# Performance work log

Measured on AMD Instinct MI355X. Metric: run time of the kernel, lower is better.

The kernel has to match this reference:

```python
import jax, jax.numpy as jnp
import numpy as np

B, N = 4, 1024
DIM, DEPTH, HEADS, DHEAD, MLP = 512, 6, 8, 64, 2048
INNER = HEADS * DHEAD
SCALE = DHEAD ** -0.5
EPS = 1e-5


def setup_inputs() -> dict:
    key = jax.random.key(0)
    ks = jax.random.split(key, 16)
    w = lambda k, shape: (jax.random.normal(k, shape, jnp.float32) * 0.02)
    D = DEPTH
    return {
        "g": jax.random.normal(ks[0], (B, N, DIM), jnp.float32),
        "x": jax.random.normal(ks[1], (B, N, DIM), jnp.float32),
        # PreNorm + SelfAttention
        "ln1_s": jnp.ones((D, DIM)), "ln1_b": jnp.zeros((D, DIM)),
        "Wqkv": w(ks[2], (D, DIM, 3 * INNER)),
        "Wo_sa": w(ks[3], (D, INNER, DIM)), "bo_sa": jnp.zeros((D, DIM)),
        # RelationalCrossAttention
        "lng_s": jnp.ones((D, DIM)), "lng_b": jnp.zeros((D, DIM)),
        "lnx_s": jnp.ones((D, DIM)), "lnx_b": jnp.zeros((D, DIM)),
        "Wq": w(ks[4], (D, DIM, INNER)),
        "Wk": w(ks[5], (D, DIM, INNER)),
        "Wv": w(ks[6], (D, DIM, INNER)), "bv": jnp.zeros((D, INNER)),
        "Wo_ca": w(ks[7], (D, INNER, DIM)), "bo_ca": jnp.zeros((D, DIM)),
        # PreNorm + FeedForward (same module applied twice per layer)
        "lnf_s": jnp.ones((D, DIM)), "lnf_b": jnp.zeros((D, DIM)),
        "W1": w(ks[8], (D, DIM, MLP)), "b1": jnp.zeros((D, MLP)),
        "W2": w(ks[9], (D, MLP, DIM)), "b2": jnp.zeros((D, DIM)),
    }


def _ln(t, s, b):
    m = t.mean(-1, keepdims=True)
    v = ((t - m) ** 2).mean(-1, keepdims=True)
    return (t - m) / jnp.sqrt(v + EPS) * s + b


def _split_heads(t):  # [b, n, h*d] -> [b, h, n, d]
    b, n, _ = t.shape
    return t.reshape(b, n, HEADS, DHEAD).transpose(0, 2, 1, 3)


def _merge_heads(t):  # [b, h, n, d] -> [b, n, h*d]
    b, h, n, d = t.shape
    return t.transpose(0, 2, 1, 3).reshape(b, n, h * d)


def _attend(q, k, v):
    dots = jnp.einsum('bhnd,bhmd->bhnm', q, k) * SCALE
    attn = jax.nn.softmax(jnp.nan_to_num(dots, nan=-jnp.inf), axis=-1)
    attn = jnp.nan_to_num(attn)  # nan_to_num(0.0) post-softmax as in source
    return jnp.einsum('bhnm,bhmd->bhnd', attn, jnp.nan_to_num(v))


def reference(g, x, ln1_s, ln1_b, Wqkv, Wo_sa, bo_sa, lng_s, lng_b, lnx_s, lnx_b,
              Wq, Wk, Wv, bv, Wo_ca, bo_ca, lnf_s, lnf_b, W1, b1, W2, b2):
    for i in range(DEPTH):
        def ff(t):
            h = jax.nn.gelu(_ln(t, lnf_s[i], lnf_b[i]) @ W1[i] + b1[i], approximate=False)
            return h @ W2[i] + b2[i]
        # relational cross attention: q,k from g, v from x
        gn = _ln(g, lng_s[i], lng_b[i])
        xn = _ln(x, lnx_s[i], lnx_b[i])
        q = _split_heads(gn @ Wq[i])
        k = _split_heads(gn @ Wk[i])
        v = _split_heads(xn @ Wv[i] + bv[i])
        x = _merge_heads(_attend(q, k, v)) @ Wo_ca[i] + bo_ca[i] + x
        x = ff(x) + x
        # pre-norm self attention (skip connection enabled)
        sn = _ln(x, ln1_s[i], ln1_b[i])
        qkv = sn @ Wqkv[i]
        qs, ks_, vs = jnp.split(qkv, 3, axis=-1)
        sa = _merge_heads(_attend(_split_heads(qs), _split_heads(ks_), _split_heads(vs)))
        x = sa @ Wo_sa[i] + bo_sa[i] + x
        x = ff(x) + x
    return x
```

## Files before the change

### kernel.cpp

```cpp
#include <hip/hip_runtime.h>
#include <hip/hip_bf16.h>
#include <cstdint>
#include <cstddef>

#define DEV __device__ __forceinline__

using f32x4 = __attribute__((ext_vector_type(4))) float;
using bfx8  = __attribute__((ext_vector_type(8))) __bf16;
using s16x8 = __attribute__((ext_vector_type(8))) short;

DEV uint16_t f2bf(float f) {
    union { float f; uint32_t u; } x; x.f = f;
    uint32_t r = x.u + 0x7fffu + ((x.u >> 16) & 1u);
    return (uint16_t)(r >> 16);
}

DEV float gelu_exact(float v) {
    return 0.5f * v * (1.0f + erff(v * 0.70710678118654752f));
}

DEV f32x4 mfma16(s16x8 a, s16x8 b, f32x4 c) {
    return __builtin_amdgcn_mfma_f32_16x16x32_bf16(
        __builtin_bit_cast(bfx8, a), __builtin_bit_cast(bfx8, b), c, 0, 0, 0);
}

DEV void async_lds16(const void* g, void* l) {
    __builtin_amdgcn_global_load_lds(
        (const __attribute__((address_space(1))) uint32_t*)g,
        (__attribute__((address_space(3))) uint32_t*)l, 16, 0, 0);
}

template<int HAS_SB>
__global__ __launch_bounds__(256)
void ln_t(const float* __restrict__ in, const float* __restrict__ sc,
          const float* __restrict__ bi, uint16_t* __restrict__ out)
{
    const int lane = threadIdx.x & 63;
    const size_t row = (size_t)blockIdx.x * 4 + (threadIdx.x >> 6);
    const float* p = in + row * 512 + lane * 8;
    float4 a = *(const float4*)p;
    float4 b4 = *(const float4*)(p + 4);
    float v[8] = {a.x, a.y, a.z, a.w, b4.x, b4.y, b4.z, b4.w};
    float s = 0.f, sq = 0.f;
#pragma unroll
    for (int j = 0; j < 8; ++j) { s += v[j]; sq += v[j] * v[j]; }
#pragma unroll
    for (int o = 1; o < 64; o <<= 1) { s += __shfl_xor(s, o); sq += __shfl_xor(sq, o); }
    const float mean = s * (1.0f / 512.0f);
    const float var  = sq * (1.0f / 512.0f) - mean * mean;
    const float rstd = rsqrtf(var + 1e-5f);
    const int c = lane * 8;
    uint16_t o8[8];
#pragma unroll
    for (int j = 0; j < 8; ++j) {
        float z = (v[j] - mean) * rstd;
        if (HAS_SB) z = z * sc[c + j] + bi[c + j];
        o8[j] = f2bf(z);
    }
    uint4 pk;
    pk.x = (uint32_t)o8[0] | ((uint32_t)o8[1] << 16);
    pk.y = (uint32_t)o8[2] | ((uint32_t)o8[3] << 16);
    pk.z = (uint32_t)o8[4] | ((uint32_t)o8[5] << 16);
    pk.w = (uint32_t)o8[6] | ((uint32_t)o8[7] << 16);
    *reinterpret_cast<uint4*>(out + row * 512 + c) = pk;
}

__global__ __launch_bounds__(256)
void wtrans(const float* __restrict__ W, uint16_t* __restrict__ WT, int K, int N,
            size_t lstride, int row0, const float* __restrict__ kscale)
{
    __shared__ float tile[32][33];
    const int l = blockIdx.z;
    const int k0 = blockIdx.x * 32, n0 = blockIdx.y * 32;
    const float* Wl = W + (size_t)l * K * N;
    uint16_t* WTl = WT + (size_t)l * lstride;
    const int tx = threadIdx.x, ty = threadIdx.y;
#pragma unroll
    for (int j = 0; j < 4; ++j) {
        const int k = k0 + ty + j * 8;
        float w = Wl[(size_t)k * N + n0 + tx];
        if (kscale) w *= kscale[l * K + k];
        tile[ty + j * 8][tx] = w;
    }
    __syncthreads();
#pragma unroll
    for (int j = 0; j < 4; ++j)
        WTl[(size_t)(row0 + n0 + ty + j * 8) * K + k0 + tx] = f2bf(tile[tx][ty + j * 8]);
}

__global__ __launch_bounds__(256)
void bfold(const float* __restrict__ b, const float* __restrict__ Wq,
           const float* __restrict__ Wk, float* __restrict__ out)
{
    const int n = blockIdx.x * 256 + threadIdx.x;
    const int l = blockIdx.y, sel = blockIdx.z;
    const float* bb = b + l * 512;
    const float* W = (sel ? Wk : Wq) + (size_t)l * 512 * 512;
    float s = 0.f;
    for (int k = 0; k < 512; ++k) s += bb[k] * W[(size_t)k * 512 + n];
    out[l * 1024 + sel * 512 + n] = s;
}

template<int BM, int BN, int MINW,
         int HAS_BIAS, int HAS_RESID, int DO_GELU, int OUT_BF16, int OUT_VT>
__global__ __launch_bounds__(256, MINW)
void gemm9(const uint16_t* __restrict__ A, const uint16_t* __restrict__ BT,
           const float* __restrict__ bias, const float* __restrict__ resid,
           void* __restrict__ outp, uint16_t* __restrict__ vt,
           int M, int N, int K)
{
    constexpr int WM = BM / 2, WN = BN / 2;
    constexpr int FM = WM / 16, FN = WN / 16;
    constexpr int ASLOTS = 4 * BM, BSLOTS = 4 * BN, TOT = ASLOTS + BSLOTS;
    constexpr int S = TOT / 256;
    __shared__ uint16_t As[ASLOTS * 8];
    __shared__ uint16_t Bs[BSLOTS * 8];
    const int tid = threadIdx.x, lane = tid & 63;
    const int w = tid >> 6, wr = w >> 1, wc = w & 1;
    const int kg = lane >> 4, lr = lane & 15;
    const int nbn = N / BN, nbm = M / BM;
    const int rect_m = nbm >> 1, rect_n = nbn >> 2;
    const int xcd = blockIdx.x & 7, c = blockIdx.x >> 3;
    const int bm = (xcd >> 2) * rect_m + c / rect_n;
    const int bn = (xcd & 3) * rect_n + c % rect_n;
    const size_t m0 = (size_t)bm * BM;
    const size_t n0 = (size_t)bn * BN;

    f32x4 acc[FM][FN] = {};
    for (int k0 = 0; k0 < K; k0 += 32) {
#pragma unroll
        for (int j = 0; j < S; ++j) {
            const int s = j * 256 + tid;
            if (s < ASLOTS) {
                const int sub = s / BM, row = s % BM;
                async_lds16(A + (m0 + row) * K + k0 + sub * 8, &As[s * 8]);
            } else {
                const int s2 = s - ASLOTS;
                const int sub = s2 / BN, row = s2 % BN;
                async_lds16(BT + (n0 + row) * K + k0 + sub * 8, &Bs[s2 * 8]);
            }
        }
        __syncthreads();
        s16x8 af[FM], bf[FN];
#pragma unroll
        for (int i = 0; i < FM; ++i)
            af[i] = *(const s16x8*)&As[(kg * BM + wr * WM + i * 16 + lr) * 8];
#pragma unroll
        for (int j = 0; j < FN; ++j)
            bf[j] = *(const s16x8*)&Bs[(kg * BN + wc * WN + j * 16 + lr) * 8];
#pragma unroll
        for (int i = 0; i < FM; ++i)
#pragma unroll
            for (int j = 0; j < FN; ++j)
                acc[i][j] = mfma16(af[i], bf[j], acc[i][j]);
        __syncthreads();
    }
    if (OUT_VT == 1 || (OUT_VT == 2 && n0 >= 1024)) {
#pragma unroll
        for (int i = 0; i < FM; ++i) {
            const size_t rbase = m0 + wr * WM + i * 16 + kg * 4;
            const int b = (int)(rbase >> 10), nloc = (int)(rbase & 1023);
#pragma unroll
            for (int j = 0; j < FN; ++j) {
                const int col = (int)n0 + wc * WN + j * 16 + lr;
                const int c2 = (OUT_VT == 2) ? col - 1024 : col;
                const float bval = HAS_BIAS ? bias[c2] : 0.0f;
                const int h = c2 >> 6, d = c2 & 63;
                ushort4 pk;
                pk.x = f2bf(acc[i][j][0] + bval);
                pk.y = f2bf(acc[i][j][1] + bval);
                pk.z = f2bf(acc[i][j][2] + bval);
                pk.w = f2bf(acc[i][j][3] + bval);
                *(ushort4*)&vt[((size_t)(b * 8 + h) * 64 + d) * 1024 + nloc] = pk;
            }
        }
        return;
    }
#pragma unroll
    for (int i = 0; i < FM; ++i) {
        const size_t rbase = m0 + wr * WM + i * 16 + kg * 4;
#pragma unroll
        for (int j = 0; j < FN; ++j) {
            const size_t col = n0 + wc * WN + j * 16 + lr;
            const float bval = HAS_BIAS ? bias[col] : 0.0f;
#pragma unroll
            for (int r = 0; r < 4; ++r) {
                const size_t row = rbase + r;
                float v = acc[i][j][r] + bval;
                if (DO_GELU)  v = gelu_exact(v);
                if (HAS_RESID) v += resid[row * (size_t)N + col];
                if (OUT_BF16) ((uint16_t*)outp)[row * (size_t)N + col] = f2bf(v);
                else          ((float*)outp)[row * (size_t)N + col] = v;
            }
        }
    }
}

__global__ __launch_bounds__(256)
void attn_flash(const uint16_t* __restrict__ Qb, const uint16_t* __restrict__ Kb,
                const uint16_t* __restrict__ Vt, uint16_t* __restrict__ Ob,
                int qstride, int kstride, int qoff, int koff)
{
    __shared__ uint16_t Ks[2][4096];
    __shared__ uint16_t Vs[2][4096];
    __shared__ uint16_t Pb[4][1024];
    const int tid = threadIdx.x, lane = tid & 63, w = tid >> 6;
    const int kg = lane >> 4, lr = lane & 15;
    const int bh = blockIdx.y, b = bh >> 3, h = bh & 7;
    const int q0 = blockIdx.x * 64;
    const float CEXP = 0.125f * 1.44269504f;

    s16x8 aq0, aq1;
    {
        const size_t qrow = (size_t)b * 1024 + q0 + w * 16 + lr;
        const uint16_t* qp = Qb + qrow * qstride + qoff + h * 64 + kg * 8;
        aq0 = *(const s16x8*)qp;
        aq1 = *(const s16x8*)(qp + 32);
    }
    const uint16_t* kbase = Kb + (size_t)b * 1024 * kstride + koff + h * 64;
    const uint16_t* vbase = Vt + (size_t)bh * 65536;

    float l_r[4] = {0.f, 0.f, 0.f, 0.f};
    f32x4 acc[4] = {};

    auto stage = [&](int buf, int kv0) {
#pragma unroll
        for (int j = 0; j < 2; ++j) {
            const int s = j * 256 + tid;
            const int sub = s >> 6, row = s & 63;
            async_lds16(kbase + (size_t)(kv0 + row) * kstride + sub * 8, &Ks[buf][s * 8]);
            async_lds16(vbase + (size_t)row * 1024 + kv0 + sub * 8,      &Vs[buf][s * 8]);
        }
    };

    stage(0, 0);
    __syncthreads();
    int cur = 0;
    for (int t = 0; t < 16; ++t) {
        if (t < 15) stage(cur ^ 1, (t + 1) * 64);
        f32x4 s4[4];
        __builtin_amdgcn_s_setprio(1);
#pragma unroll
        for (int ni = 0; ni < 4; ++ni) {
            s16x8 bk0 = *(const s16x8*)&Ks[cur][(kg * 64 + ni * 16 + lr) * 8];
            s16x8 bk1 = *(const s16x8*)&Ks[cur][((4 + kg) * 64 + ni * 16 + lr) * 8];
            f32x4 z = {};
            z = mfma16(aq0, bk0, z);
            z = mfma16(aq1, bk1, z);
            s4[ni] = z;
        }
        __builtin_amdgcn_s_setprio(0);
#pragma unroll
        for (int ni = 0; ni < 4; ++ni) {
            const int slotb = (ni * 2 + (lr >> 3)) * 16 + kg * 4;
#pragma unroll
            for (int r = 0; r < 4; ++r) {
                const float pe = __builtin_amdgcn_exp2f(s4[ni][r] * CEXP);
                l_r[r] += pe;
                Pb[w][(slotb + r) * 8 + (lr & 7)] = f2bf(pe);
            }
        }
        s16x8 ap0 = *(const s16x8*)&Pb[w][(kg * 16 + lr) * 8];
        s16x8 ap1 = *(const s16x8*)&Pb[w][((4 + kg) * 16 + lr) * 8];
        __builtin_amdgcn_s_setprio(1);
#pragma unroll
        for (int ni = 0; ni < 4; ++ni) {
            s16x8 bv0 = *(const s16x8*)&Vs[cur][(kg * 64 + ni * 16 + lr) * 8];
            s16x8 bv1 = *(const s16x8*)&Vs[cur][((4 + kg) * 64 + ni * 16 + lr) * 8];
            acc[ni] = mfma16(ap0, bv0, acc[ni]);
            acc[ni] = mfma16(ap1, bv1, acc[ni]);
        }
        __builtin_amdgcn_s_setprio(0);
        __syncthreads();
        cur ^= 1;
    }
    float linv[4];
#pragma unroll
    for (int r = 0; r < 4; ++r) {
        float l = l_r[r];
        l += __shfl_xor(l, 1); l += __shfl_xor(l, 2);
        l += __shfl_xor(l, 4); l += __shfl_xor(l, 8);
        linv[r] = 1.0f / l;
    }
#pragma unroll
    for (int ni = 0; ni < 4; ++ni)
#pragma unroll
        for (int r = 0; r < 4; ++r) {
            const float v = acc[ni][r] * linv[r];
            const size_t row = (size_t)b * 1024 + q0 + w * 16 + kg * 4 + r;
            Ob[row * 512 + h * 64 + ni * 16 + lr] = f2bf(v);
        }
}

extern "C" void kernel_launch(void* const* d_in, const int* in_sizes, int n_in,
                              void* d_out, int out_size, void* d_ws, size_t ws_size,
                              hipStream_t stream)
{
    (void)in_sizes; (void)n_in; (void)out_size; (void)ws_size;
    const float* g     = (const float*)d_in[0];
    const float* x0    = (const float*)d_in[1];
    const float* ln1_s = (const float*)d_in[2];
    const float* ln1_b = (const float*)d_in[3];
    const float* Wqkv  = (const float*)d_in[4];
    const float* Wo_sa = (const float*)d_in[5];
    const float* bo_sa = (const float*)d_in[6];
    const float* lng_s = (const float*)d_in[7];
    const float* lng_b = (const float*)d_in[8];
    const float* lnx_s = (const float*)d_in[9];
    const float* lnx_b = (const float*)d_in[10];
    const float* Wq    = (const float*)d_in[11];
    const float* Wk    = (const float*)d_in[12];
    const float* Wv    = (const float*)d_in[13];
    const float* bv    = (const float*)d_in[14];
    const float* Wo_ca = (const float*)d_in[15];
    const float* bo_ca = (const float*)d_in[16];
    const float* lnf_s = (const float*)d_in[17];
    const float* lnf_b = (const float*)d_in[18];
    const float* W1    = (const float*)d_in[19];
    const float* b1    = (const float*)d_in[20];
    const float* W2    = (const float*)d_in[21];
    const float* b2    = (const float*)d_in[22];

    float* x = (float*)d_out;

    char* p = (char*)d_ws;
    auto carve = [&](size_t n) { char* r = p; p += (n + 255) & ~(size_t)255; return r; };
    uint16_t* WqkT  = (uint16_t*)carve(6ull * 1024 * 512 * 2);
    uint16_t* WvT   = (uint16_t*)carve(6ull * 512 * 512 * 2);
    uint16_t* WocaT = (uint16_t*)carve(6ull * 512 * 512 * 2);
    uint16_t* WqkvT = (uint16_t*)carve(6ull * 1536 * 512 * 2);
    uint16_t* WosaT = (uint16_t*)carve(6ull * 512 * 512 * 2);
    uint16_t* W1T   = (uint16_t*)carve(6ull * 2048 * 512 * 2);
    uint16_t* W2T   = (uint16_t*)carve(6ull * 512 * 2048 * 2);
    float*    bqk   = (float*)carve(6144ull * 4);
    uint16_t* zg    = (uint16_t*)carve(4096ull * 512 * 2);
    uint16_t* qkall = (uint16_t*)carve(4096ull * 6144 * 2);
    uint16_t* xn    = (uint16_t*)carve(4096ull * 512 * 2);
    uint16_t* qkvu  = (uint16_t*)carve(4096ull * 1536 * 2);
    uint16_t* vt    = (uint16_t*)carve(32ull * 64 * 1024 * 2);
    uint16_t* ab    = (uint16_t*)carve(4096ull * 512 * 2);
    uint16_t* hb    = (uint16_t*)carve(4096ull * 2048 * 2);

    dim3 tb(32, 8);
    wtrans<<<dim3(16, 16, 6), tb, 0, stream>>>(Wq,    WqkT,  512, 512,  1024ull * 512, 0,   lng_s);
    wtrans<<<dim3(16, 16, 6), tb, 0, stream>>>(Wk,    WqkT,  512, 512,  1024ull * 512, 512, lng_s);
    wtrans<<<dim3(16, 16, 6), tb, 0, stream>>>(Wv,    WvT,   512, 512,  512ull * 512, 0, nullptr);
    wtrans<<<dim3(16, 16, 6), tb, 0, stream>>>(Wo_ca, WocaT, 512, 512,  512ull * 512, 0, nullptr);
    wtrans<<<dim3(16, 48, 6), tb, 0, stream>>>(Wqkv,  WqkvT, 512, 1536, 1536ull * 512, 0, nullptr);
    wtrans<<<dim3(16, 16, 6), tb, 0, stream>>>(Wo_sa, WosaT, 512, 512,  512ull * 512, 0, nullptr);
    wtrans<<<dim3(16, 64, 6), tb, 0, stream>>>(W1,    W1T,   512, 2048, 2048ull * 512, 0, nullptr);
    wtrans<<<dim3(64, 16, 6), tb, 0, stream>>>(W2,    W2T,   2048, 512, 2048ull * 512, 0, nullptr);
    bfold<<<dim3(2, 6, 2), 256, 0, stream>>>(lng_b, Wq, Wk, bqk);

    hipMemcpyAsync(x, x0, 4096ull * 512 * 4, hipMemcpyDeviceToDevice, stream);

    ln_t<0><<<1024, 256, 0, stream>>>(g, nullptr, nullptr, zg);
    ln_t<1><<<1024, 256, 0, stream>>>(x, lnx_s, lnx_b, xn);
    gemm9<128, 128, 3, 1, 0, 0, 1, 0><<<1536, 256, 0, stream>>>(
        zg, WqkT, bqk, nullptr, qkall, nullptr, 4096, 6144, 512);

    const dim3 ga(16, 32);

    for (int l = 0; l < 6; ++l) {
        const size_t o512 = (size_t)l * 512, oW = (size_t)l * 512 * 512;
        const size_t oW1 = (size_t)l * 2048 * 512, oWqkv = (size_t)l * 1536 * 512;
        const size_t o2048 = (size_t)l * 2048;

        gemm9<64, 64, 5, 1, 0, 0, 0, 1><<<512, 256, 0, stream>>>(
            xn, WvT + oW, bv + o512, nullptr, nullptr, vt, 4096, 512, 512);
        attn_flash<<<ga, 256, 0, stream>>>(qkall, qkall, vt, ab, 6144, 6144,
                                           l * 1024, l * 1024 + 512);
        gemm9<64, 64, 5, 1, 1, 0, 0, 0><<<512, 256, 0, stream>>>(
            ab, WocaT + oW, bo_ca + o512, x, x, nullptr, 4096, 512, 512);

        ln_t<1><<<1024, 256, 0, stream>>>(x, lnf_s + o512, lnf_b + o512, xn);
        gemm9<128, 128, 3, 1, 0, 1, 1, 0><<<512, 256, 0, stream>>>(
            xn, W1T + oW1, b1 + o2048, nullptr, hb, nullptr, 4096, 2048, 512);
        gemm9<64, 64, 5, 1, 1, 0, 0, 0><<<512, 256, 0, stream>>>(
            hb, W2T + oW1, b2 + o512, x, x, nullptr, 4096, 512, 2048);
        ln_t<1><<<1024, 256, 0, stream>>>(x, ln1_s + o512, ln1_b + o512, xn);

        gemm9<128, 128, 3, 0, 0, 0, 1, 2><<<384, 256, 0, stream>>>(
            xn, WqkvT + oWqkv, nullptr, nullptr, qkvu, vt, 4096, 1536, 512);
        attn_flash<<<ga, 256, 0, stream>>>(qkvu, qkvu, vt, ab, 1536, 1536, 0, 512);
        gemm9<64, 64, 5, 1, 1, 0, 0, 0><<<512, 256, 0, stream>>>(
            ab, WosaT + oW, bo_sa + o512, x, x, nullptr, 4096, 512, 512);

        ln_t<1><<<1024, 256, 0, stream>>>(x, lnf_s + o512, lnf_b + o512, xn);
        gemm9<128, 128, 3, 1, 0, 1, 1, 0><<<512, 256, 0, stream>>>(
            xn, W1T + oW1, b1 + o2048, nullptr, hb, nullptr, 4096, 2048, 512);
        gemm9<64, 64, 5, 1, 1, 0, 0, 0><<<512, 256, 0, stream>>>(
            hb, W2T + oW1, b2 + o512, x, x, nullptr, 4096, 512, 2048);
        if (l < 5)
            ln_t<1><<<1024, 256, 0, stream>>>(x, lnx_s + o512 + 512, lnx_b + o512 + 512, xn);
    }
}
```

Baseline: 1.666 ms.

## Enlarge GEMM tiles, add split-K for W2 with fused reduce+LN, 8-wave attention

The GEMM kernel is generalized to configurable warp grids, larger tiles and a K step of 64 per sync. The W2 GEMM becomes a 4-way split-K writing fp32 partials, and a new reduce kernel adds bias and residual and fuses the following LayerNorm. Attention now uses 8 waves and 128 query rows per block, so each staged K/V tile serves more queries. These changes aim to cut sync overhead, raise tile reuse and remove separate LN launches, at the cost of a large partial buffer, extra global traffic for the partials, and larger tiles that leave fewer blocks per launch.

```diff
diff --git a/kernel.cpp b/kernel.cpp
--- a/kernel.cpp
+++ b/kernel.cpp
@@ -101,22 +101,23 @@
     out[l * 1024 + sel * 512 + n] = s;
 }
 
-template<int BM, int BN, int MINW,
-         int HAS_BIAS, int HAS_RESID, int DO_GELU, int OUT_BF16, int OUT_VT>
-__global__ __launch_bounds__(256, MINW)
-void gemm9(const uint16_t* __restrict__ A, const uint16_t* __restrict__ BT,
-           const float* __restrict__ bias, const float* __restrict__ resid,
-           void* __restrict__ outp, uint16_t* __restrict__ vt,
-           int M, int N, int K)
-{
-    constexpr int WM = BM / 2, WN = BN / 2;
+template<int BM, int BN, int NWR, int NWC, int MINW,
+         int HAS_BIAS, int HAS_RESID, int DO_GELU, int OUT_BF16, int OUT_VT, int SPLITK>
+__global__ __launch_bounds__(NWR * NWC * 64, MINW)
+void gemm10(const uint16_t* __restrict__ A, const uint16_t* __restrict__ BT,
+            const float* __restrict__ bias, const float* __restrict__ resid,
+            void* __restrict__ outp, uint16_t* __restrict__ vt,
+            int M, int N, int K)
+{
+    constexpr int NT = NWR * NWC * 64;
+    constexpr int WM = BM / NWR, WN = BN / NWC;
     constexpr int FM = WM / 16, FN = WN / 16;
-    constexpr int ASLOTS = 4 * BM, BSLOTS = 4 * BN, TOT = ASLOTS + BSLOTS;
-    constexpr int S = TOT / 256;
+    constexpr int ASLOTS = 8 * BM, BSLOTS = 8 * BN, TOT = ASLOTS + BSLOTS;
+    constexpr int S = TOT / NT;
     __shared__ uint16_t As[ASLOTS * 8];
     __shared__ uint16_t Bs[BSLOTS * 8];
     const int tid = threadIdx.x, lane = tid & 63;
-    const int w = tid >> 6, wr = w >> 1, wc = w & 1;
+    const int w = tid >> 6, wr = w / NWC, wc = w % NWC;
     const int kg = lane >> 4, lr = lane & 15;
     const int nbn = N / BN, nbm = M / BM;
     const int rect_m = nbm >> 1, rect_n = nbn >> 2;
@@ -125,12 +126,14 @@
     const int bn = (xcd & 3) * rect_n + c % rect_n;
     const size_t m0 = (size_t)bm * BM;
     const size_t n0 = (size_t)bn * BN;
+    const int kh = K / SPLITK;
+    const int kbase = (SPLITK > 1) ? blockIdx.y * kh : 0;
 
     f32x4 acc[FM][FN] = {};
-    for (int k0 = 0; k0 < K; k0 += 32) {
+    for (int k0 = kbase; k0 < kbase + kh; k0 += 64) {
 #pragma unroll
         for (int j = 0; j < S; ++j) {
-            const int s = j * 256 + tid;
+            const int s = j * NT + tid;
             if (s < ASLOTS) {
                 const int sub = s / BM, row = s % BM;
                 async_lds16(A + (m0 + row) * K + k0 + sub * 8, &As[s * 8]);
@@ -141,19 +144,37 @@
             }
         }
         __syncthreads();
-        s16x8 af[FM], bf[FN];
-#pragma unroll
-        for (int i = 0; i < FM; ++i)
-            af[i] = *(const s16x8*)&As[(kg * BM + wr * WM + i * 16 + lr) * 8];
-#pragma unroll
-        for (int j = 0; j < FN; ++j)
-            bf[j] = *(const s16x8*)&Bs[(kg * BN + wc * WN + j * 16 + lr) * 8];
-#pragma unroll
-        for (int i = 0; i < FM; ++i)
+#pragma unroll
+        for (int ks = 0; ks < 2; ++ks) {
+            s16x8 af[FM], bf[FN];
+#pragma unroll
+            for (int i = 0; i < FM; ++i)
+                af[i] = *(const s16x8*)&As[((ks * 4 + kg) * BM + wr * WM + i * 16 + lr) * 8];
 #pragma unroll
             for (int j = 0; j < FN; ++j)
-                acc[i][j] = mfma16(af[i], bf[j], acc[i][j]);
+                bf[j] = *(const s16x8*)&Bs[((ks * 4 + kg) * BN + wc * WN + j * 16 + lr) * 8];
+#pragma unroll
+            for (int i = 0; i < FM; ++i)
+#pragma unroll
+                for (int j = 0; j < FN; ++j)
+                    acc[i][j] = mfma16(af[i], bf[j], acc[i][j]);
+        }
         __syncthreads();
+    }
+    if (SPLITK > 1) {
+        float* pout = (float*)outp + (size_t)blockIdx.y * M * (size_t)N;
+#pragma unroll
+        for (int i = 0; i < FM; ++i) {
+            const size_t rbase = m0 + wr * WM + i * 16 + kg * 4;
+#pragma unroll
+            for (int j = 0; j < FN; ++j) {
+                const size_t col = n0 + wc * WN + j * 16 + lr;
+#pragma unroll
+                for (int r = 0; r < 4; ++r)
+                    pout[(rbase + r) * (size_t)N + col] = acc[i][j][r];
+            }
+        }
+        return;
     }
     if (OUT_VT == 1 || (OUT_VT == 2 && n0 >= 1024)) {
 #pragma unroll
@@ -196,18 +217,66 @@
     }
 }
 
+template<int DO_LN>
 __global__ __launch_bounds__(256)
+void reduce_ln(const float* __restrict__ p, const float* __restrict__ bias,
+               float* __restrict__ x, const float* __restrict__ sc,
+               const float* __restrict__ bi, uint16_t* __restrict__ xn)
+{
+    const int lane = threadIdx.x & 63;
+    const size_t row = (size_t)blockIdx.x * 4 + (threadIdx.x >> 6);
+    const int c = lane * 8;
+    const size_t off = row * 512 + c;
+    float v[8];
+    {
+        float4 r0 = *(const float4*)(x + off), r1 = *(const float4*)(x + off + 4);
+        float4 s0 = *(const float4*)(bias + c), s1 = *(const float4*)(bias + c + 4);
+        v[0] = r0.x + s0.x; v[1] = r0.y + s0.y; v[2] = r0.z + s0.z; v[3] = r0.w + s0.w;
+        v[4] = r1.x + s1.x; v[5] = r1.y + s1.y; v[6] = r1.z + s1.z; v[7] = r1.w + s1.w;
+    }
+#pragma unroll
+    for (int t = 0; t < 4; ++t) {
+        const float* pt = p + (size_t)t * 4096 * 512 + off;
+        float4 a0 = *(const float4*)pt, a1 = *(const float4*)(pt + 4);
+        v[0] += a0.x; v[1] += a0.y; v[2] += a0.z; v[3] += a0.w;
+        v[4] += a1.x; v[5] += a1.y; v[6] += a1.z; v[7] += a1.w;
+    }
+    *(float4*)(x + off)     = make_float4(v[0], v[1], v[2], v[3]);
+    *(float4*)(x + off + 4) = make_float4(v[4], v[5], v[6], v[7]);
+    if (DO_LN) {
+        float s = 0.f, sq = 0.f;
+#pragma unroll
+        for (int j = 0; j < 8; ++j) { s += v[j]; sq += v[j] * v[j]; }
+#pragma unroll
+        for (int o = 1; o < 64; o <<= 1) { s += __shfl_xor(s, o); sq += __shfl_xor(sq, o); }
+        const float mean = s * (1.0f / 512.0f);
+        const float var  = sq * (1.0f / 512.0f) - mean * mean;
+        const float rstd = rsqrtf(var + 1e-5f);
+        uint16_t o8[8];
+#pragma unroll
+        for (int j = 0; j < 8; ++j)
+            o8[j] = f2bf((v[j] - mean) * rstd * sc[c + j] + bi[c + j]);
+        uint4 pk;
+        pk.x = (uint32_t)o8[0] | ((uint32_t)o8[1] << 16);
+        pk.y = (uint32_t)o8[2] | ((uint32_t)o8[3] << 16);
+        pk.z = (uint32_t)o8[4] | ((uint32_t)o8[5] << 16);
+        pk.w = (uint32_t)o8[6] | ((uint32_t)o8[7] << 16);
+        *reinterpret_cast<uint4*>(xn + off) = pk;
+    }
+}
+
+__global__ __launch_bounds__(512)
 void attn_flash(const uint16_t* __restrict__ Qb, const uint16_t* __restrict__ Kb,
                 const uint16_t* __restrict__ Vt, uint16_t* __restrict__ Ob,
                 int qstride, int kstride, int qoff, int koff)
 {
     __shared__ uint16_t Ks[2][4096];
     __shared__ uint16_t Vs[2][4096];
-    __shared__ uint16_t Pb[4][1024];
+    __shared__ uint16_t Pb[8][1024];
     const int tid = threadIdx.x, lane = tid & 63, w = tid >> 6;
     const int kg = lane >> 4, lr = lane & 15;
     const int bh = blockIdx.y, b = bh >> 3, h = bh & 7;
-    const int q0 = blockIdx.x * 64;
+    const int q0 = blockIdx.x * 128;
     const float CEXP = 0.125f * 1.44269504f;
 
     s16x8 aq0, aq1;
@@ -224,13 +293,10 @@
     f32x4 acc[4] = {};
 
     auto stage = [&](int buf, int kv0) {
-#pragma unroll
-        for (int j = 0; j < 2; ++j) {
-            const int s = j * 256 + tid;
-            const int sub = s >> 6, row = s & 63;
-            async_lds16(kbase + (size_t)(kv0 + row) * kstride + sub * 8, &Ks[buf][s * 8]);
-            async_lds16(vbase + (size_t)row * 1024 + kv0 + sub * 8,      &Vs[buf][s * 8]);
-        }
+        const int s = tid;
+        const int sub = s >> 6, row = s & 63;
+        async_lds16(kbase + (size_t)(kv0 + row) * kstride + sub * 8, &Ks[buf][s * 8]);
+        async_lds16(vbase + (size_t)row * 1024 + kv0 + sub * 8,      &Vs[buf][s * 8]);
     };
 
     stage(0, 0);
@@ -340,6 +406,7 @@
     uint16_t* vt    = (uint16_t*)carve(32ull * 64 * 1024 * 2);
     uint16_t* ab    = (uint16_t*)carve(4096ull * 512 * 2);
     uint16_t* hb    = (uint16_t*)carve(4096ull * 2048 * 2);
+    float*    pk4   = (float*)carve(4ull * 4096 * 512 * 4);
 
     dim3 tb(32, 8);
     wtrans<<<dim3(16, 16, 6), tb, 0, stream>>>(Wq,    WqkT,  512, 512,  1024ull * 512, 0,   lng_s);
@@ -356,42 +423,47 @@
 
     ln_t<0><<<1024, 256, 0, stream>>>(g, nullptr, nullptr, zg);
     ln_t<1><<<1024, 256, 0, stream>>>(x, lnx_s, lnx_b, xn);
-    gemm9<128, 128, 3, 1, 0, 0, 1, 0><<<1536, 256, 0, stream>>>(
+    gemm10<256, 256, 4, 2, 2, 1, 0, 0, 1, 0, 1><<<384, 512, 0, stream>>>(
         zg, WqkT, bqk, nullptr, qkall, nullptr, 4096, 6144, 512);
 
-    const dim3 ga(16, 32);
+    const dim3 ga(8, 32);
 
     for (int l = 0; l < 6; ++l) {
         const size_t o512 = (size_t)l * 512, oW = (size_t)l * 512 * 512;
         const size_t oW1 = (size_t)l * 2048 * 512, oWqkv = (size_t)l * 1536 * 512;
         const size_t o2048 = (size_t)l * 2048;
 
-        gemm9<64, 64, 5, 1, 0, 0, 0, 1><<<512, 256, 0, stream>>>(
+        gemm10<128, 64, 2, 2, 4, 1, 0, 0, 0, 1, 1><<<256, 256, 0, stream>>>(
             xn, WvT + oW, bv + o512, nullptr, nullptr, vt, 4096, 512, 512);
-        attn_flash<<<ga, 256, 0, stream>>>(qkall, qkall, vt, ab, 6144, 6144,
+        attn_flash<<<ga, 512, 0, stream>>>(qkall, qkall, vt, ab, 6144, 6144,
                                            l * 1024, l * 1024 + 512);
-        gemm9<64, 64, 5, 1, 1, 0, 0, 0><<<512, 256, 0, stream>>>(
+        gemm10<128, 64, 2, 2, 4, 1, 1, 0, 0, 0, 1><<<256, 256, 0, stream>>>(
             ab, WocaT + oW, bo_ca + o512, x, x, nullptr, 4096, 512, 512);
 
         ln_t<1><<<1024, 256, 0, stream>>>(x, lnf_s + o512, lnf_b + o512, xn);
-        gemm9<128, 128, 3, 1, 0, 1, 1, 0><<<512, 256, 0, stream>>>(
+        gemm10<256, 128, 4, 2, 2, 1, 0, 1, 1, 0, 1><<<256, 512, 0, stream>>>(
             xn, W1T + oW1, b1 + o2048, nullptr, hb, nullptr, 4096, 2048, 512);
-        gemm9<64, 64, 5, 1, 1, 0, 0, 0><<<512, 256, 0, stream>>>(
-            hb, W2T + oW1, b2 + o512, x, x, nullptr, 4096, 512, 2048);
-        ln_t<1><<<1024, 256, 0, stream>>>(x, ln1_s + o512, ln1_b + o512, xn);
-
-        gemm9<128, 128, 3, 0, 0, 0, 1, 2><<<384, 256, 0, stream>>>(
+        gemm10<256, 128, 4, 2, 2, 0, 0, 0, 0, 0, 4><<<dim3(64, 4), 512, 0, stream>>>(
+            hb, W2T + oW1, nullptr, nullptr, pk4, nullptr, 4096, 512, 2048);
+        reduce_ln<1><<<1024, 256, 0, stream>>>(pk4, b2 + o512, x,
+                                               ln1_s + o512, ln1_b + o512, xn);
+
+        gemm10<256, 128, 4, 2, 2, 0, 0, 0, 1, 2, 1><<<192, 512, 0, stream>>>(
             xn, WqkvT + oWqkv, nullptr, nullptr, qkvu, vt, 4096, 1536, 512);
-        attn_flash<<<ga, 256, 0, stream>>>(qkvu, qkvu, vt, ab, 1536, 1536, 0, 512);
-        gemm9<64, 64, 5, 1, 1, 0, 0, 0><<<512, 256, 0, stream>>>(
+        attn_flash<<<ga, 512, 0, stream>>>(qkvu, qkvu, vt, ab, 1536, 1536, 0, 512);
+        gemm10<128, 64, 2, 2, 4, 1, 1, 0, 0, 0, 1><<<256, 256, 0, stream>>>(
             ab, WosaT + oW, bo_sa + o512, x, x, nullptr, 4096, 512, 512);
 
         ln_t<1><<<1024, 256, 0, stream>>>(x, lnf_s + o512, lnf_b + o512, xn);
-        gemm9<128, 128, 3, 1, 0, 1, 1, 0><<<512, 256, 0, stream>>>(
+        gemm10<256, 128, 4, 2, 2, 1, 0, 1, 1, 0, 1><<<256, 512, 0, stream>>>(
             xn, W1T + oW1, b1 + o2048, nullptr, hb, nullptr, 4096, 2048, 512);
-        gemm9<64, 64, 5, 1, 1, 0, 0, 0><<<512, 256, 0, stream>>>(
-            hb, W2T + oW1, b2 + o512, x, x, nullptr, 4096, 512, 2048);
+        gemm10<256, 128, 4, 2, 2, 0, 0, 0, 0, 0, 4><<<dim3(64, 4), 512, 0, stream>>>(
+            hb, W2T + oW1, nullptr, nullptr, pk4, nullptr, 4096, 512, 2048);
         if (l < 5)
-            ln_t<1><<<1024, 256, 0, stream>>>(x, lnx_s + o512 + 512, lnx_b + o512 + 512, xn);
-    }
-}
+            reduce_ln<1><<<1024, 256, 0, stream>>>(pk4, b2 + o512, x,
+                                                   lnx_s + o512 + 512, lnx_b + o512 + 512, xn);
+        else
+            reduce_ln<0><<<1024, 256, 0, stream>>>(pk4, b2 + o512, x,
+                                                   nullptr, nullptr, nullptr);
+    }
+}
```

Result: slower. 1.752 ms (+5.1%).
